# Optimization experiments

Hardware: AMD Instinct MI355X
Metric: run time of the kernel (lower is better)

Reference implementation:

```python
import jax, jax.numpy as jnp
import numpy as np

B, S, I, H = 1024, 512, 1, 50  # batch, seq_len, input_size, hidden_size


def setup_inputs() -> dict:
    key = jax.random.key(0)
    ks = jax.random.split(key, 7)
    s_ih = 1.0 / np.sqrt(H)
    return {
        "x": jax.random.normal(ks[0], (B, S, I), dtype=jnp.float32),
        "h0": jnp.zeros((1, B, H), dtype=jnp.float32),
        "c0": jnp.zeros((1, B, H), dtype=jnp.float32),
        # PyTorch nn.LSTM params, gate order [i, f, g, o]
        "W_ih": jax.random.uniform(ks[1], (4 * H, I), jnp.float32, -s_ih, s_ih),
        "W_hh": jax.random.uniform(ks[2], (4 * H, H), jnp.float32, -s_ih, s_ih),
        "b_ih": jax.random.uniform(ks[3], (4 * H,), jnp.float32, -s_ih, s_ih),
        "b_hh": jax.random.uniform(ks[4], (4 * H,), jnp.float32, -s_ih, s_ih),
        "fc_w": jax.random.uniform(ks[5], (1, H), jnp.float32, -s_ih, s_ih),
        "fc_b": jax.random.uniform(ks[6], (1,), jnp.float32, -s_ih, s_ih),
    }


def reference(x, h0, c0, W_ih, W_hh, b_ih, b_hh, fc_w, fc_b):
    # Precompute the input projection for all timesteps: [B, S, 4H] -> scan over S
    x_proj = jnp.einsum("bsi,gi->bsg", x, W_ih) + (b_ih + b_hh)
    x_proj = jnp.transpose(x_proj, (1, 0, 2))  # [S, B, 4H]

    def step(carry, xp_t):
        h, c = carry  # each [B, H]
        gates = xp_t + h @ W_hh.T  # [B, 4H]
        i_g, f_g, g_g, o_g = jnp.split(gates, 4, axis=-1)
        c_new = jax.nn.sigmoid(f_g) * c + jax.nn.sigmoid(i_g) * jnp.tanh(g_g)
        h_new = jax.nn.sigmoid(o_g) * jnp.tanh(c_new)
        return (h_new, c_new), None

    (h_n, c_n), _ = jax.lax.scan(step, (h0[0], c0[0]), x_proj)
    # out[:, -1, :] is the final hidden state; fc head: [B, H] -> [B, 1]
    out = h_n @ fc_w.T + fc_b
    return out, h_n[None], c_n[None]
```

## Files before the change

### kernel.cpp

```cpp
#include <hip/hip_runtime.h>


typedef _Float16 half2v __attribute__((ext_vector_type(2)));

#define LOG2E 1.44269504088896340736f
#define B_ 1024
#define S_ 512
#define H_ 50

__device__ __forceinline__ float rcp_(float x) { return __builtin_amdgcn_rcpf(x); }
__device__ __forceinline__ float ex2_(float x) { return __builtin_amdgcn_exp2f(x); }

__global__ void lstm_pack(const float* __restrict__ W_ih, const float* __restrict__ W_hh,
                          const float* __restrict__ b_ih, const float* __restrict__ b_hh,
                          unsigned* __restrict__ wpk, float* __restrict__ wih_pk,
                          float* __restrict__ bias_pk)
{
    int tid = blockIdx.x * blockDim.x + threadIdx.x;
    int stride = blockDim.x * gridDim.x;
    for (int p = tid; p < 4 * 25 * 64; p += stride) {
        int j = p & 63;
        int m = (p >> 6) % 25;
        int g = p / (25 * 64);
        float s = (g == 2) ? (2.0f * LOG2E) : (-LOG2E);
        float a = 0.0f, bb = 0.0f;
        if (j < H_) {
            int row = g * H_ + j;
            a  = s * W_hh[row * H_ + 2 * m];
            bb = s * W_hh[row * H_ + 2 * m + 1];
        }
        half2v hv;
        hv.x = (_Float16)a;
        hv.y = (_Float16)bb;
        wpk[p] = __builtin_bit_cast(unsigned, hv);
    }
    for (int p = tid; p < 4 * 64; p += stride) {
        int j = p & 63;
        int g = p >> 6;
        float s = (g == 2) ? (2.0f * LOG2E) : (-LOG2E);
        float wi = 0.0f, bb = 0.0f;
        if (j < H_) {
            int row = g * H_ + j;
            wi = s * W_ih[row];
            bb = s * (b_ih[row] + b_hh[row]);
        }
        wih_pk[p] = wi;
        bias_pk[p] = bb;
    }
}

__global__ __launch_bounds__(64, 1) void lstm_main(
    const float* __restrict__ x, const float* __restrict__ h0, const float* __restrict__ c0,
    const float* __restrict__ fc_w, const float* __restrict__ fc_b,
    const unsigned* __restrict__ wpk, const float* __restrict__ wih_pk,
    const float* __restrict__ bias_pk, float* __restrict__ out)
{
    const int b = blockIdx.x;
    const int j = threadIdx.x;

    int xr[S_ / 64];
    #pragma unroll
    for (int t = 0; t < S_ / 64; ++t)
        xr[t] = __builtin_bit_cast(int, x[b * S_ + 64 * t + j]);

    half2v w0[25], w1[25], w2[25], w3[25];
    #pragma unroll
    for (int m = 0; m < 25; ++m) {
        w0[m] = __builtin_bit_cast(half2v, wpk[(0 * 25 + m) * 64 + j]);
        w1[m] = __builtin_bit_cast(half2v, wpk[(1 * 25 + m) * 64 + j]);
        w2[m] = __builtin_bit_cast(half2v, wpk[(2 * 25 + m) * 64 + j]);
        w3[m] = __builtin_bit_cast(half2v, wpk[(3 * 25 + m) * 64 + j]);
    }
    float wih0 = wih_pk[0 * 64 + j], wih1 = wih_pk[1 * 64 + j];
    float wih2 = wih_pk[2 * 64 + j], wih3 = wih_pk[3 * 64 + j];
    float bs0 = bias_pk[0 * 64 + j], bs1 = bias_pk[1 * 64 + j];
    float bs2 = bias_pk[2 * 64 + j], bs3 = bias_pk[3 * 64 + j];

    float h = (j < H_) ? h0[b * H_ + j] : 0.0f;
    float c = (j < H_) ? c0[b * H_ + j] : 0.0f;

    int hn_ = __builtin_amdgcn_update_dpp(0, __builtin_bit_cast(int, h),
                                          0xB1, 0xF, 0xF, true);
    unsigned hpk = __builtin_bit_cast(unsigned,
        __builtin_amdgcn_cvt_pkrtz(h, __builtin_bit_cast(float, hn_)));

    for (int s = 0; s < S_; ++s) {
        float xt = __builtin_bit_cast(float,
            __builtin_amdgcn_readlane(xr[s >> 6], s & 63));
        float aA0 = __builtin_fmaf(xt, wih0, bs0);
        float aA1 = __builtin_fmaf(xt, wih1, bs1);
        float aA2 = __builtin_fmaf(xt, wih2, bs2);
        float aA3 = __builtin_fmaf(xt, wih3, bs3);
        float aB0 = 0.0f, aB1 = 0.0f, aB2 = 0.0f, aB3 = 0.0f;

        #pragma unroll
        for (int m = 0; m < 25; ++m) {
            unsigned um = (unsigned)__builtin_amdgcn_readlane((int)hpk, 2 * m);
            half2v hm = __builtin_bit_cast(half2v, um);
            if (m & 1) {
                aB0 = __builtin_amdgcn_fdot2(hm, w0[m], aB0, false);
                aB1 = __builtin_amdgcn_fdot2(hm, w1[m], aB1, false);
                aB2 = __builtin_amdgcn_fdot2(hm, w2[m], aB2, false);
                aB3 = __builtin_amdgcn_fdot2(hm, w3[m], aB3, false);
            } else {
                aA0 = __builtin_amdgcn_fdot2(hm, w0[m], aA0, false);
                aA1 = __builtin_amdgcn_fdot2(hm, w1[m], aA1, false);
                aA2 = __builtin_amdgcn_fdot2(hm, w2[m], aA2, false);
                aA3 = __builtin_amdgcn_fdot2(hm, w3[m], aA3, false);
            }
        }
        float a0 = aA0 + aB0;
        float a1 = aA1 + aB1;
        float a2 = aA2 + aB2;
        float a3 = aA3 + aB3;

        float ei = ex2_(a0); float si = rcp_(1.0f + ei);
        float ef = ex2_(a1); float sf = rcp_(1.0f + ef);
        float eg = ex2_(a2);
        float tg = __builtin_fmaf(-2.0f, rcp_(1.0f + eg), 1.0f);
        float eo = ex2_(a3); float so = rcp_(1.0f + eo);

        c = __builtin_fmaf(sf, c, si * tg);
        float ec = ex2_((2.0f * LOG2E) * c);
        float tc = __builtin_fmaf(-2.0f, rcp_(1.0f + ec), 1.0f);
        h = so * tc;

        int hnn_ = __builtin_amdgcn_update_dpp(0, __builtin_bit_cast(int, h),
                                               0xB1, 0xF, 0xF, true);
        hpk = __builtin_bit_cast(unsigned,
            __builtin_amdgcn_cvt_pkrtz(h, __builtin_bit_cast(float, hnn_)));
    }

    if (j < H_) {
        out[B_ + b * H_ + j]            = h;
        out[B_ + B_ * H_ + b * H_ + j]  = c;
    }
    float p = (j < H_) ? h * fc_w[j] : 0.0f;
    #pragma unroll
    for (int off = 32; off > 0; off >>= 1) p += __shfl_xor(p, off);
    if (j == 0) out[b] = p + fc_b[0];
}

extern "C" void kernel_launch(void* const* d_in, const int* in_sizes, int n_in,
                              void* d_out, int out_size, void* d_ws, size_t ws_size,
                              hipStream_t stream)
{
    const float* x    = (const float*)d_in[0];
    const float* h0   = (const float*)d_in[1];
    const float* c0   = (const float*)d_in[2];
    const float* W_ih = (const float*)d_in[3];
    const float* W_hh = (const float*)d_in[4];
    const float* b_ih = (const float*)d_in[5];
    const float* b_hh = (const float*)d_in[6];
    const float* fc_w = (const float*)d_in[7];
    const float* fc_b = (const float*)d_in[8];
    float* out = (float*)d_out;

    unsigned* wpk  = (unsigned*)d_ws;
    float* wih_pk  = (float*)((char*)d_ws + 6400 * 4);
    float* bias_pk = (float*)((char*)d_ws + 6400 * 4 + 256 * 4);

    lstm_pack<<<16, 256, 0, stream>>>(W_ih, W_hh, b_ih, b_hh, wpk, wih_pk, bias_pk);
    lstm_main<<<B_, 64, 0, stream>>>(x, h0, c0, fc_w, fc_b, wpk, wih_pk, bias_pk, out);
}
```

Before: 199.9 us.

## Broadcast packed hidden state via LDS instead of per-element readlane

Replaces the 25 serialized v_readlane broadcasts of the packed fp16 hidden state with a single LDS write by even lanes followed by 25 LDS reads into registers. It also drops the split A/B accumulator chains for single accumulators and prefetches x one step ahead from global memory instead of holding it in registers. The goal is to shorten the per-step serial latency of the recurrence. The cost is LDS round-trip latency, with no explicit barrier in a single-wave block, longer dependent fdot2 chains, and a global load on each step.

```diff
diff --git a/kernel.cpp b/kernel.cpp
--- a/kernel.cpp
+++ b/kernel.cpp
@@ -49,19 +49,19 @@
     }
 }
 
-__global__ __launch_bounds__(64, 1) void lstm_main(
-    const float* __restrict__ x, const float* __restrict__ h0, const float* __restrict__ c0,
-    const float* __restrict__ fc_w, const float* __restrict__ fc_b,
-    const unsigned* __restrict__ wpk, const float* __restrict__ wih_pk,
-    const float* __restrict__ bias_pk, float* __restrict__ out)
+__global__
+__attribute__((amdgpu_flat_work_group_size(64, 64)))
+__attribute__((amdgpu_waves_per_eu(1, 1)))
+void lstm_main(const float* __restrict__ x, const float* __restrict__ h0,
+               const float* __restrict__ c0, const float* __restrict__ fc_w,
+               const float* __restrict__ fc_b, const unsigned* __restrict__ wpk,
+               const float* __restrict__ wih_pk, const float* __restrict__ bias_pk,
+               float* __restrict__ out)
 {
     const int b = blockIdx.x;
     const int j = threadIdx.x;
 
-    int xr[S_ / 64];
-    #pragma unroll
-    for (int t = 0; t < S_ / 64; ++t)
-        xr[t] = __builtin_bit_cast(int, x[b * S_ + 64 * t + j]);
+    __shared__ unsigned hs16[32];
 
     half2v w0[25], w1[25], w2[25], w3[25];
     #pragma unroll
@@ -71,6 +71,7 @@
         w2[m] = __builtin_bit_cast(half2v, wpk[(2 * 25 + m) * 64 + j]);
         w3[m] = __builtin_bit_cast(half2v, wpk[(3 * 25 + m) * 64 + j]);
     }
+
     float wih0 = wih_pk[0 * 64 + j], wih1 = wih_pk[1 * 64 + j];
     float wih2 = wih_pk[2 * 64 + j], wih3 = wih_pk[3 * 64 + j];
     float bs0 = bias_pk[0 * 64 + j], bs1 = bias_pk[1 * 64 + j];
@@ -79,41 +80,37 @@
     float h = (j < H_) ? h0[b * H_ + j] : 0.0f;
     float c = (j < H_) ? c0[b * H_ + j] : 0.0f;
 
-    int hn_ = __builtin_amdgcn_update_dpp(0, __builtin_bit_cast(int, h),
-                                          0xB1, 0xF, 0xF, true);
-    unsigned hpk = __builtin_bit_cast(unsigned,
-        __builtin_amdgcn_cvt_pkrtz(h, __builtin_bit_cast(float, hn_)));
+    {
+        int hn_ = __builtin_amdgcn_update_dpp(0, __builtin_bit_cast(int, h),
+                                              0xB1, 0xF, 0xF, true);
+        unsigned hpk = __builtin_bit_cast(unsigned,
+            __builtin_amdgcn_cvt_pkrtz(h, __builtin_bit_cast(float, hn_)));
+        if ((j & 1) == 0 && j < H_ + 1) hs16[j >> 1] = hpk;
+    }
+    unsigned hp[25];
+    #pragma unroll
+    for (int m = 0; m < 25; ++m) hp[m] = hs16[m];
+
+    const float* __restrict__ xrow = x + b * S_;
+    float xt = xrow[0];
 
     for (int s = 0; s < S_; ++s) {
-        float xt = __builtin_bit_cast(float,
-            __builtin_amdgcn_readlane(xr[s >> 6], s & 63));
-        float aA0 = __builtin_fmaf(xt, wih0, bs0);
-        float aA1 = __builtin_fmaf(xt, wih1, bs1);
-        float aA2 = __builtin_fmaf(xt, wih2, bs2);
-        float aA3 = __builtin_fmaf(xt, wih3, bs3);
-        float aB0 = 0.0f, aB1 = 0.0f, aB2 = 0.0f, aB3 = 0.0f;
+        int sn = s + 1 < S_ ? s + 1 : S_ - 1;
+        float xt_n = xrow[sn];
+
+        float a0 = __builtin_fmaf(xt, wih0, bs0);
+        float a1 = __builtin_fmaf(xt, wih1, bs1);
+        float a2 = __builtin_fmaf(xt, wih2, bs2);
+        float a3 = __builtin_fmaf(xt, wih3, bs3);
 
         #pragma unroll
         for (int m = 0; m < 25; ++m) {
-            unsigned um = (unsigned)__builtin_amdgcn_readlane((int)hpk, 2 * m);
-            half2v hm = __builtin_bit_cast(half2v, um);
-            if (m & 1) {
-                aB0 = __builtin_amdgcn_fdot2(hm, w0[m], aB0, false);
-                aB1 = __builtin_amdgcn_fdot2(hm, w1[m], aB1, false);
-                aB2 = __builtin_amdgcn_fdot2(hm, w2[m], aB2, false);
-                aB3 = __builtin_amdgcn_fdot2(hm, w3[m], aB3, false);
-            } else {
-                aA0 = __builtin_amdgcn_fdot2(hm, w0[m], aA0, false);
-                aA1 = __builtin_amdgcn_fdot2(hm, w1[m], aA1, false);
-                aA2 = __builtin_amdgcn_fdot2(hm, w2[m], aA2, false);
-                aA3 = __builtin_amdgcn_fdot2(hm, w3[m], aA3, false);
-            }
+            half2v hm = __builtin_bit_cast(half2v, hp[m]);
+            a0 = __builtin_amdgcn_fdot2(hm, w0[m], a0, false);
+            a1 = __builtin_amdgcn_fdot2(hm, w1[m], a1, false);
+            a2 = __builtin_amdgcn_fdot2(hm, w2[m], a2, false);
+            a3 = __builtin_amdgcn_fdot2(hm, w3[m], a3, false);
         }
-        float a0 = aA0 + aB0;
-        float a1 = aA1 + aB1;
-        float a2 = aA2 + aB2;
-        float a3 = aA3 + aB3;
-
         float ei = ex2_(a0); float si = rcp_(1.0f + ei);
         float ef = ex2_(a1); float sf = rcp_(1.0f + ef);
         float eg = ex2_(a2);
@@ -125,10 +122,15 @@
         float tc = __builtin_fmaf(-2.0f, rcp_(1.0f + ec), 1.0f);
         h = so * tc;
 
-        int hnn_ = __builtin_amdgcn_update_dpp(0, __builtin_bit_cast(int, h),
-                                               0xB1, 0xF, 0xF, true);
-        hpk = __builtin_bit_cast(unsigned,
-            __builtin_amdgcn_cvt_pkrtz(h, __builtin_bit_cast(float, hnn_)));
+        int hn_ = __builtin_amdgcn_update_dpp(0, __builtin_bit_cast(int, h),
+                                              0xB1, 0xF, 0xF, true);
+        unsigned hpk = __builtin_bit_cast(unsigned,
+            __builtin_amdgcn_cvt_pkrtz(h, __builtin_bit_cast(float, hn_)));
+        if ((j & 1) == 0 && j < H_ + 1) hs16[j >> 1] = hpk;
+        #pragma unroll
+        for (int m = 0; m < 25; ++m) hp[m] = hs16[m];
+
+        xt = xt_n;
     }
 
     if (j < H_) {
```

Result: no change. 198.3 us (-0.8%).
